# Kernel tuning notes

Hardware: AMD Instinct MI355X
Metric: run time of the kernel (lower is better)

## Reference

```python
import jax, jax.numpy as jnp
import numpy as np

B, C, H, W = 4, 256, 64, 64
C8 = C // 8


def setup_inputs() -> dict:
    key = jax.random.key(0)
    ks = jax.random.split(key, 8)
    s = 1.0 / np.sqrt(C)
    return {
        "x_ccd": jax.random.normal(ks[0], (B, C, H, W), jnp.float32),
        "x_dem": jax.random.normal(ks[1], (B, C, H, W), jnp.float32),
        "Wq": jax.random.normal(ks[2], (C8, C), jnp.float32) * s,
        "bq": jax.random.normal(ks[3], (C8,), jnp.float32) * 0.01,
        "Wk": jax.random.normal(ks[4], (C8, C), jnp.float32) * s,
        "bk": jax.random.normal(ks[5], (C8,), jnp.float32) * 0.01,
        "Wv": jax.random.normal(ks[6], (C, C), jnp.float32) * s,
        "bv": jax.random.normal(ks[7], (C,), jnp.float32) * 0.01,
        "gamma": jnp.zeros((1,), jnp.float32),
    }


def reference(x_ccd, x_dem, Wq, bq, Wk, bk, Wv, bv, gamma):
    b, c, h, w = x_ccd.shape
    n = h * w
    xc = x_ccd.reshape(b, c, n)  # [B,C,N]
    xd = x_dem.reshape(b, c, n)
    # 1x1 convs == per-pixel linear projections
    q = jnp.einsum("oc,bcn->bno", Wq, xc) + bq  # [B,N,C8]
    k = jnp.einsum("oc,bcn->bon", Wk, xd) + bk[None, :, None]  # [B,C8,N]
    energy = jnp.einsum("bno,bom->bnm", q, k)  # [B,N,N]
    attention = jax.nn.softmax(energy, axis=-1)
    v = jnp.einsum("oc,bcn->bon", Wv, xd) + bv[None, :, None]  # [B,C,N]
    out = jnp.einsum("bom,bnm->bon", v, attention)  # value @ attention^T
    out = out.reshape(b, c, h, w)
    return gamma * out + x_ccd
```

## Files before the change

### kernel.cpp

```cpp
#include <hip/hip_runtime.h>

typedef unsigned short u16;
typedef unsigned int u32;
typedef short v8s __attribute__((ext_vector_type(8)));
typedef float v16f __attribute__((ext_vector_type(16)));
typedef unsigned int v2u __attribute__((ext_vector_type(2)));

#define MFMA(a, b, c) __builtin_amdgcn_mfma_f32_32x32x16_bf16(a, b, c, 0, 0, 0)
#define L2E 1.44269504088896f

union U8 { v8s s; uint4 u4; u32 u[4]; };

__device__ __forceinline__ u16 f2bf(float x) {
    u32 u = __float_as_uint(x);
    return (u16)((u + 0x7FFFu + ((u >> 16) & 1u)) >> 16);
}
__device__ __forceinline__ u32 pk2(float a, float b) {
    return (u32)f2bf(a) | ((u32)f2bf(b) << 16);
}
__device__ __forceinline__ u32 pkz(float e0, float e1) {
    return __builtin_amdgcn_perm(__float_as_uint(e1), __float_as_uint(e0), 0x07060302u);
}


__global__ __launch_bounds__(256) void prep_w_kernel(
    const float* __restrict__ Wq, const float* __restrict__ bq,
    const float* __restrict__ Wk, const float* __restrict__ bk,
    const float* __restrict__ Wv, const float* __restrict__ bv,
    u16* __restrict__ WfT, float* __restrict__ ball)
{
    int tid = blockIdx.x * 256 + threadIdx.x;
    if (tid < 81920) {
        int ch = tid >> 8, c = tid & 255;
        float w;
        if (ch < 32)      w = Wq[ch * 256 + c];
        else if (ch < 64) w = Wk[(ch - 32) * 256 + c] * L2E;
        else              w = Wv[(ch - 64) * 256 + c];
        int tile = (ch >> 5) * 16 + (c >> 4);
        int lane = ((c >> 3) & 1) * 32 + (ch & 31);
        WfT[tile * 512 + lane * 8 + (c & 7)] = f2bf(w);
    } else if (tid < 82240) {
        int i = tid - 81920;
        float bb;
        if (i < 32)      bb = bq[i];
        else if (i < 64) bb = bk[i - 32] * L2E;
        else             bb = bv[i - 64];
        ball[i] = bb;
    }
}

__global__ __launch_bounds__(256, 2) void proj_kernel(
    const float* __restrict__ xc, const float* __restrict__ xd,
    const u16* __restrict__ WfT, const float* __restrict__ ball,
    u16* __restrict__ qfT, u16* __restrict__ kfT, u16* __restrict__ vfT)
{
    __shared__ u16 xls[2][32][264];
    int blk = blockIdx.x, b = blk >> 7, n0 = (blk & 127) * 32;
    int t = threadIdx.x, lane = t & 63, wv = t >> 6;
    int hl = lane >> 5, l31 = lane & 31;

#pragma unroll
    for (int p = 0; p < 4; p++) {
        int s = p * 256 + t;
        int arr = s >> 9, c4 = (s >> 3) & 63, n4s = s & 7;
        const float* src = arr ? xd : xc;
        size_t g0 = ((size_t)(b * 256 + c4 * 4)) * 4096 + n0 + n4s * 4;
        float4 r0 = *(const float4*)&src[g0];
        float4 r1 = *(const float4*)&src[g0 + 4096];
        float4 r2 = *(const float4*)&src[g0 + 8192];
        float4 r3 = *(const float4*)&src[g0 + 12288];
        *(uint2*)&xls[arr][n4s * 4 + 0][c4 * 4] = make_uint2(pk2(r0.x, r1.x), pk2(r2.x, r3.x));
        *(uint2*)&xls[arr][n4s * 4 + 1][c4 * 4] = make_uint2(pk2(r0.y, r1.y), pk2(r2.y, r3.y));
        *(uint2*)&xls[arr][n4s * 4 + 2][c4 * 4] = make_uint2(pk2(r0.z, r1.z), pk2(r2.z, r3.z));
        *(uint2*)&xls[arr][n4s * 4 + 3][c4 * 4] = make_uint2(pk2(r0.w, r1.w), pk2(r2.w, r3.w));
    }
    __syncthreads();

    int jobs[3];
    int nj;
    if (wv == 0)      { jobs[0] = 0; jobs[1] = 2; jobs[2] = 0; nj = 2; }
    else if (wv == 1) { jobs[0] = 1; jobs[1] = 3; jobs[2] = 0; nj = 2; }
    else if (wv == 2) { jobs[0] = 4; jobs[1] = 5; jobs[2] = 6; nj = 3; }
    else              { jobs[0] = 7; jobs[1] = 8; jobs[2] = 9; nj = 3; }

    int nt = blk & 127;
    int n = n0 + l31;
    int vl = ((n >> 3) & 1) * 32, tk = n >> 4, j8 = n & 7;

    for (int jj = 0; jj < nj; jj++) {
        int j = jobs[jj];
        int arr = (j != 0);
        const u16* wb = WfT + (size_t)(j * 16) * 512 + lane * 8;
        v16f acc = {};
#pragma unroll
        for (int kc = 0; kc < 16; kc++) {
            U8 bx, a;
            bx.u4 = *(const uint4*)&xls[arr][l31][kc * 16 + hl * 8];
            a.u4  = *(const uint4*)(wb + (size_t)kc * 512);
            acc = MFMA(a.s, bx.s, acc);
        }
        if (j <= 1) {
            u16* dst = j ? kfT : qfT;
#pragma unroll
            for (int i = 0; i < 8; i++) {
                int r = 2 * i;
                int row = (r & 3) + 8 * (r >> 2) + 4 * hl;
                float b0 = ball[j * 32 + row], b1 = ball[j * 32 + row + 1];
                u32 st = pk2(acc[r] + b0, acc[r + 1] + b1);
                size_t off = (((size_t)(b * 128 + nt) * 2 + (row >> 4)) * 512)
                           + (((row >> 3) & 1) * 32 + l31) * 8 + (row & 7);
                *(u32*)&dst[off] = st;
            }
        } else {
            int vi = j - 2;
            u16* vdst = vfT + (((size_t)(b * 8 + vi) * 256 + tk) * 512) + vl * 8 + j8;
#pragma unroll
            for (int r = 0; r < 16; r++) {
                int row = (r & 3) + 8 * (r >> 2) + 4 * hl;
                vdst[row * 8] = f2bf(acc[r] + ball[64 + vi * 32 + row]);
            }
        }
    }
}

union ShU {
    u32   P[2][8][2][64][4];
    float red[4][2][16][64];
};

__global__ __launch_bounds__(512, 4) void flash_kernel(
    const u16* __restrict__ qfT, const u16* __restrict__ kfT,
    const u16* __restrict__ vfT, const float* __restrict__ xccd,
    const float* __restrict__ gptr, float* __restrict__ outp)
{
    __shared__ ShU sh;
    __shared__ float lred[8][32];

    const int t = threadIdx.x, lane = t & 63, wv = t >> 6;
    const int hl = lane >> 5, l31 = lane & 31;
    const int blk = blockIdx.x;
    const int b  = (blk & 7) >> 1;
    const int qt = ((blk >> 3) << 1) | (blk & 1);
    const int kq = wv >> 2, chq = wv & 3;
    const int n0 = qt * 32;

    U8 qf0, qf1;
    {
        const u16* qp = qfT + ((size_t)(b * 128 + qt) * 2) * 512 + lane * 8;
        qf0.u4 = *(const uint4*)qp;
        qf1.u4 = *(const uint4*)(qp + 512);
    }

    v16f acc[2] = {};
    float lrun = 0.f;

    const u16* kp = kfT + ((size_t)(b * 128 + wv)) * 1024 + lane * 8;
    const u16* vp = vfT + ((size_t)(b * 8 + chq * 2) * 256) * 512 + lane * 8;

    U8 kb0[2], kb1[2];
    kb0[0].u4 = *(const uint4*)(kp);
    kb0[1].u4 = *(const uint4*)(kp + 512);
    kb1[0].u4 = *(const uint4*)(kp + 8192);
    kb1[1].u4 = *(const uint4*)(kp + 8192 + 512);

    auto produce = [&](U8 (&kb)[2], int buf) {
        v16f E = {};
        E = MFMA(kb[0].s, qf0.s, E);
        E = MFMA(kb[1].s, qf1.s, E);
        u32 pkv[8];
#pragma unroll
        for (int j = 0; j < 8; j++)
            pkv[j] = pkz(__builtin_amdgcn_exp2f(E[2 * j]),
                         __builtin_amdgcn_exp2f(E[2 * j + 1]));
        float sl = 0.f;
#pragma unroll
        for (int j = 0; j < 8; j++) {
            sl += __uint_as_float(pkv[j] & 0xFFFF0000u);
            sl += __uint_as_float(pkv[j] << 16);
        }
        lrun += sl;
        U8 B0, B1;
        v2u r;
        r = __builtin_amdgcn_permlane32_swap(pkv[0], pkv[2], 0, 0); B0.u[0] = r[0]; B0.u[2] = r[1];
        r = __builtin_amdgcn_permlane32_swap(pkv[1], pkv[3], 0, 0); B0.u[1] = r[0]; B0.u[3] = r[1];
        r = __builtin_amdgcn_permlane32_swap(pkv[4], pkv[6], 0, 0); B1.u[0] = r[0]; B1.u[2] = r[1];
        r = __builtin_amdgcn_permlane32_swap(pkv[5], pkv[7], 0, 0); B1.u[1] = r[0]; B1.u[3] = r[1];
        *(uint4*)&sh.P[buf][wv][0][lane][0] = B0.u4;
        *(uint4*)&sh.P[buf][wv][1][lane][0] = B1.u4;
    };

    produce(kb0, 0);
    __syncthreads();

    const int tb = kq * 4;
#pragma unroll 1
    for (int s = 0; s < 16; s++) {
        const int cb = s & 1, nb = cb ^ 1;
        const int t0 = s * 8 + tb;
        U8 bA0, bA1, bB0, bB1;
        bA0.u4 = *(const uint4*)&sh.P[cb][tb][0][lane][0];
        bA1.u4 = *(const uint4*)&sh.P[cb][tb][1][lane][0];
        U8 vA[2][2], vB[2][2];
        {
            const u16* v0p = vp + (size_t)(2 * t0) * 512;
            vA[0][0].u4 = *(const uint4*)(v0p);
            vA[0][1].u4 = *(const uint4*)(v0p + 512);
            vA[1][0].u4 = *(const uint4*)(v0p + 131072);
            vA[1][1].u4 = *(const uint4*)(v0p + 131072 + 512);
        }
        if (s < 15) {
            if ((s & 1) == 0) {
                produce(kb1, nb);
                if (s < 14) {
                    kb0[0].u4 = *(const uint4*)(kp + (size_t)(s + 2) * 8192);
                    kb0[1].u4 = *(const uint4*)(kp + (size_t)(s + 2) * 8192 + 512);
                }
            } else {
                produce(kb0, nb);
                if (s < 14) {
                    kb1[0].u4 = *(const uint4*)(kp + (size_t)(s + 2) * 8192);
                    kb1[1].u4 = *(const uint4*)(kp + (size_t)(s + 2) * 8192 + 512);
                }
            }
        }
#pragma unroll
        for (int j = 0; j < 4; j++) {
            if (j < 3) {
                bB0.u4 = *(const uint4*)&sh.P[cb][tb + j + 1][0][lane][0];
                bB1.u4 = *(const uint4*)&sh.P[cb][tb + j + 1][1][lane][0];
                const u16* vnp = vp + (size_t)(2 * (t0 + j + 1)) * 512;
                vB[0][0].u4 = *(const uint4*)(vnp);
                vB[0][1].u4 = *(const uint4*)(vnp + 512);
                vB[1][0].u4 = *(const uint4*)(vnp + 131072);
                vB[1][1].u4 = *(const uint4*)(vnp + 131072 + 512);
            }
            __builtin_amdgcn_s_setprio(1);
            acc[0] = MFMA(vA[0][0].s, bA0.s, acc[0]);
            acc[0] = MFMA(vA[0][1].s, bA1.s, acc[0]);
            acc[1] = MFMA(vA[1][0].s, bA0.s, acc[1]);
            acc[1] = MFMA(vA[1][1].s, bA1.s, acc[1]);
            __builtin_amdgcn_s_setprio(0);
            bA0 = bB0; bA1 = bB1;
            vA[0][0] = vB[0][0]; vA[0][1] = vB[0][1];
            vA[1][0] = vB[1][0]; vA[1][1] = vB[1][1];
        }
        __syncthreads();
    }

    {
        v2u rr = __builtin_amdgcn_permlane32_swap(__float_as_uint(lrun),
                                                  __float_as_uint(lrun), 0, 0);
        float ltot = __uint_as_float(rr[0]) + __uint_as_float(rr[1]);
        if (lane < 32) lred[wv][l31] = ltot;
    }
    if (kq == 1) {
#pragma unroll
        for (int ct = 0; ct < 2; ct++)
#pragma unroll
            for (int r = 0; r < 16; r++)
                sh.red[chq][ct][r][lane] = acc[ct][r];
    }
    __syncthreads();
    if (kq == 0) {
        float lsum = 0.f;
#pragma unroll
        for (int w = 0; w < 8; w++) lsum += lred[w][l31];
        const float g = gptr[0];
        const float sc = g / lsum;
#pragma unroll
        for (int ct = 0; ct < 2; ct++)
#pragma unroll
            for (int r = 0; r < 16; r++) {
                float v = acc[ct][r] + sh.red[chq][ct][r][lane];
                int ch = chq * 64 + ct * 32 + (r & 3) + 8 * (r >> 2) + 4 * hl;
                size_t ga = ((size_t)(b * 256 + ch)) * 4096 + n0 + l31;
                outp[ga] = v * sc + xccd[ga];
            }
    }
}

extern "C" void kernel_launch(void* const* d_in, const int* in_sizes, int n_in,
                              void* d_out, int out_size, void* d_ws, size_t ws_size,
                              hipStream_t stream)
{
    const float* xc    = (const float*)d_in[0];
    const float* xd    = (const float*)d_in[1];
    const float* Wq    = (const float*)d_in[2];
    const float* bq    = (const float*)d_in[3];
    const float* Wk    = (const float*)d_in[4];
    const float* bk    = (const float*)d_in[5];
    const float* Wv    = (const float*)d_in[6];
    const float* bv    = (const float*)d_in[7];
    const float* gamma = (const float*)d_in[8];
    float* out = (float*)d_out;

    u16* qfT  = (u16*)d_ws;
    u16* kfT  = qfT + (size_t)524288;
    u16* vfT  = kfT + (size_t)524288;
    u16* WfT  = vfT + (size_t)4194304;
    float* bl = (float*)(WfT + 81920);

    prep_w_kernel<<<322, 256, 0, stream>>>(Wq, bq, Wk, bk, Wv, bv, WfT, bl);
    proj_kernel<<<512, 256, 0, stream>>>(xc, xd, WfT, bl, qfT, kfT, vfT);
    flash_kernel<<<512, 512, 0, stream>>>(qfT, kfT, vfT, xc, gamma, out);
}
```

Measured before the change: 155.1 us.

## Repartition flash PV work: waves own 128 channels over 2 key tiles

Changes the per-wave split of the P·V accumulation. Each wave previously covered 64 channels over 4 key tiles per step; it now covers 128 channels (4 accumulators) over 2 key tiles per step. Each P fragment read from shared memory is reused across more channels, and each wave issues 8 MFMAs per tile instead of 4. The cost is more accumulator registers and a longer final reduction, now 3 serialized shared-memory passes with extra barriers instead of one. The higher register count also puts occupancy at risk under launch_bounds(512,4).

```diff
diff --git a/kernel.cpp b/kernel.cpp
--- a/kernel.cpp
+++ b/kernel.cpp
@@ -125,7 +125,7 @@
 
 union ShU {
     u32   P[2][8][2][64][4];
-    float red[4][2][16][64];
+    float red[2][4][16][64];
 };
 
 __global__ __launch_bounds__(512, 4) void flash_kernel(
@@ -141,7 +141,7 @@
     const int blk = blockIdx.x;
     const int b  = (blk & 7) >> 1;
     const int qt = ((blk >> 3) << 1) | (blk & 1);
-    const int kq = wv >> 2, chq = wv & 3;
+    const int chh = wv & 1, kq = wv >> 1;
     const int n0 = qt * 32;
 
     U8 qf0, qf1;
@@ -151,11 +151,11 @@
         qf1.u4 = *(const uint4*)(qp + 512);
     }
 
-    v16f acc[2] = {};
+    v16f acc[4] = {};
     float lrun = 0.f;
 
     const u16* kp = kfT + ((size_t)(b * 128 + wv)) * 1024 + lane * 8;
-    const u16* vp = vfT + ((size_t)(b * 8 + chq * 2) * 256) * 512 + lane * 8;
+    const u16* vp = vfT + ((size_t)(b * 8 + chh * 4) * 256) * 512 + lane * 8;
 
     U8 kb0[2], kb1[2];
     kb0[0].u4 = *(const uint4*)(kp);
@@ -192,21 +192,22 @@
     produce(kb0, 0);
     __syncthreads();
 
-    const int tb = kq * 4;
+    const int tl0 = kq * 2 + chh;
+    const int tl1 = kq * 2 + (chh ^ 1);
+
 #pragma unroll 1
     for (int s = 0; s < 16; s++) {
         const int cb = s & 1, nb = cb ^ 1;
-        const int t0 = s * 8 + tb;
+        const int T0 = s * 8 + tl0, T1 = s * 8 + tl1;
         U8 bA0, bA1, bB0, bB1;
-        bA0.u4 = *(const uint4*)&sh.P[cb][tb][0][lane][0];
-        bA1.u4 = *(const uint4*)&sh.P[cb][tb][1][lane][0];
-        U8 vA[2][2], vB[2][2];
-        {
-            const u16* v0p = vp + (size_t)(2 * t0) * 512;
-            vA[0][0].u4 = *(const uint4*)(v0p);
-            vA[0][1].u4 = *(const uint4*)(v0p + 512);
-            vA[1][0].u4 = *(const uint4*)(v0p + 131072);
-            vA[1][1].u4 = *(const uint4*)(v0p + 131072 + 512);
+        bA0.u4 = *(const uint4*)&sh.P[cb][tl0][0][lane][0];
+        bA1.u4 = *(const uint4*)&sh.P[cb][tl0][1][lane][0];
+        U8 vA[4][2], vB[4][2];
+#pragma unroll
+        for (int c = 0; c < 4; c++) {
+            const u16* q = vp + (size_t)c * 131072 + (size_t)(2 * T0) * 512;
+            vA[c][0].u4 = *(const uint4*)(q);
+            vA[c][1].u4 = *(const uint4*)(q + 512);
         }
         if (s < 15) {
             if ((s & 1) == 0) {
@@ -223,27 +224,28 @@
                 }
             }
         }
-#pragma unroll
-        for (int j = 0; j < 4; j++) {
-            if (j < 3) {
-                bB0.u4 = *(const uint4*)&sh.P[cb][tb + j + 1][0][lane][0];
-                bB1.u4 = *(const uint4*)&sh.P[cb][tb + j + 1][1][lane][0];
-                const u16* vnp = vp + (size_t)(2 * (t0 + j + 1)) * 512;
-                vB[0][0].u4 = *(const uint4*)(vnp);
-                vB[0][1].u4 = *(const uint4*)(vnp + 512);
-                vB[1][0].u4 = *(const uint4*)(vnp + 131072);
-                vB[1][1].u4 = *(const uint4*)(vnp + 131072 + 512);
-            }
-            __builtin_amdgcn_s_setprio(1);
-            acc[0] = MFMA(vA[0][0].s, bA0.s, acc[0]);
-            acc[0] = MFMA(vA[0][1].s, bA1.s, acc[0]);
-            acc[1] = MFMA(vA[1][0].s, bA0.s, acc[1]);
-            acc[1] = MFMA(vA[1][1].s, bA1.s, acc[1]);
-            __builtin_amdgcn_s_setprio(0);
-            bA0 = bB0; bA1 = bB1;
-            vA[0][0] = vB[0][0]; vA[0][1] = vB[0][1];
-            vA[1][0] = vB[1][0]; vA[1][1] = vB[1][1];
-        }
+        bB0.u4 = *(const uint4*)&sh.P[cb][tl1][0][lane][0];
+        bB1.u4 = *(const uint4*)&sh.P[cb][tl1][1][lane][0];
+#pragma unroll
+        for (int c = 0; c < 4; c++) {
+            const u16* q = vp + (size_t)c * 131072 + (size_t)(2 * T1) * 512;
+            vB[c][0].u4 = *(const uint4*)(q);
+            vB[c][1].u4 = *(const uint4*)(q + 512);
+        }
+        __builtin_amdgcn_s_setprio(1);
+#pragma unroll
+        for (int c = 0; c < 4; c++) {
+            acc[c] = MFMA(vA[c][0].s, bA0.s, acc[c]);
+            acc[c] = MFMA(vA[c][1].s, bA1.s, acc[c]);
+        }
+        __builtin_amdgcn_s_setprio(0);
+        __builtin_amdgcn_s_setprio(1);
+#pragma unroll
+        for (int c = 0; c < 4; c++) {
+            acc[c] = MFMA(vB[c][0].s, bB0.s, acc[c]);
+            acc[c] = MFMA(vB[c][1].s, bB1.s, acc[c]);
+        }
+        __builtin_amdgcn_s_setprio(0);
         __syncthreads();
     }
 
@@ -253,14 +255,25 @@
         float ltot = __uint_as_float(rr[0]) + __uint_as_float(rr[1]);
         if (lane < 32) lred[wv][l31] = ltot;
     }
-    if (kq == 1) {
-#pragma unroll
-        for (int ct = 0; ct < 2; ct++)
-#pragma unroll
-            for (int r = 0; r < 16; r++)
-                sh.red[chq][ct][r][lane] = acc[ct][r];
-    }
-    __syncthreads();
+#pragma unroll 1
+    for (int r = 1; r < 4; r++) {
+        if (kq == r) {
+#pragma unroll
+            for (int ct = 0; ct < 4; ct++)
+#pragma unroll
+                for (int rg = 0; rg < 16; rg++)
+                    sh.red[chh][ct][rg][lane] = acc[ct][rg];
+        }
+        __syncthreads();
+        if (kq == 0) {
+#pragma unroll
+            for (int ct = 0; ct < 4; ct++)
+#pragma unroll
+                for (int rg = 0; rg < 16; rg++)
+                    acc[ct][rg] += sh.red[chh][ct][rg][lane];
+        }
+        __syncthreads();
+    }
     if (kq == 0) {
         float lsum = 0.f;
 #pragma unroll
@@ -268,13 +281,12 @@
         const float g = gptr[0];
         const float sc = g / lsum;
 #pragma unroll
-        for (int ct = 0; ct < 2; ct++)
-#pragma unroll
-            for (int r = 0; r < 16; r++) {
-                float v = acc[ct][r] + sh.red[chq][ct][r][lane];
-                int ch = chq * 64 + ct * 32 + (r & 3) + 8 * (r >> 2) + 4 * hl;
+        for (int ct = 0; ct < 4; ct++)
+#pragma unroll
+            for (int rg = 0; rg < 16; rg++) {
+                int ch = chh * 128 + ct * 32 + (rg & 3) + 8 * (rg >> 2) + 4 * hl;
                 size_t ga = ((size_t)(b * 256 + ch)) * 4096 + n0 + l31;
-                outp[ga] = v * sc + xccd[ga];
+                outp[ga] = acc[ct][rg] * sc + xccd[ga];
             }
     }
 }
```

Result: slower. 308.8 us (+99.1%).
